# Optimization experiments

Hardware: AMD Instinct MI355X
Metric: run time of the kernel (lower is better)

## Reference

```python
import jax, jax.numpy as jnp
import numpy as np

SEQ_LEN = 2_097_152  # free sequence dimension
NUM_SYMBOLS = 10
NUM_STATES = 10
NUM_CLASSES = 2


def setup_inputs() -> dict:
    key = jax.random.key(0)
    k1, k2, k3, k4 = jax.random.split(key, 4)
    # x[t] is a probability distribution over symbols (soft one-hot), matching
    # the automaton semantics and keeping the 2M-step recurrence numerically stable.
    x = jax.random.uniform(k1, (SEQ_LEN, NUM_SYMBOLS), dtype=jnp.float32)
    x = x / jnp.sum(x, axis=1, keepdims=True)
    # Parameters, initialized exactly as in the torch module (__init__ softmaxes).
    P = jax.nn.softmax(jax.random.normal(k2, (NUM_SYMBOLS, NUM_STATES, NUM_STATES), dtype=jnp.float32), axis=2)
    start_state = jax.nn.softmax(jax.random.normal(k3, (NUM_STATES,), dtype=jnp.float32), axis=0)
    accept_states = jax.nn.softmax(jax.random.normal(k4, (NUM_STATES, NUM_CLASSES), dtype=jnp.float32), axis=1)
    return {"x": x, "P": P, "start_state": start_state, "accept_states": accept_states}


def reference(x, P, start_state, accept_states):
    # Sequential recurrence: s_{t+1} = s_t @ (sum_k x[t,k] * P[k])
    def step(s, xt):
        Wt = jnp.einsum('k,kij->ij', xt, P)  # [S, S] symbol-weighted transition
        return s @ Wt, None
    s, _ = jax.lax.scan(step, start_state, x)
    return s @ accept_states  # [num_classes]
```

## Files before the change

kernel.cpp:

```cpp
#include <hip/hip_runtime.h>

#define TEN 10

typedef float v2f __attribute__((ext_vector_type(2)));

#define PK_MUL_S0LO(d,s0,s1)   asm("v_pk_mul_f32 %0, %1, %2 op_sel:[0,0] op_sel_hi:[0,1]"         : "=v"(d)  : "v"(s0), "v"(s1))
#define PK_FMA_S0LO(acc,s0,s1) asm("v_pk_fma_f32 %0, %1, %2, %0 op_sel:[0,0,0] op_sel_hi:[0,1,1]" : "+v"(acc) : "v"(s0), "v"(s1))
#define PK_FMA_S0HI(acc,s0,s1) asm("v_pk_fma_f32 %0, %1, %2, %0 op_sel:[1,0,0] op_sel_hi:[1,1,1]" : "+v"(acc) : "v"(s0), "v"(s1))
#define PK_MUL_S1LO(d,s0,s1)   asm("v_pk_mul_f32 %0, %1, %2 op_sel:[0,0] op_sel_hi:[1,0]"         : "=v"(d)  : "v"(s0), "v"(s1))
#define PK_MUL_S1HI(d,s0,s1)   asm("v_pk_mul_f32 %0, %1, %2 op_sel:[0,1] op_sel_hi:[1,1]"         : "=v"(d)  : "v"(s0), "v"(s1))
#define PK_FMA_S1LO(acc,s0,s1) asm("v_pk_fma_f32 %0, %1, %2, %0 op_sel:[0,0,0] op_sel_hi:[1,0,1]" : "+v"(acc) : "v"(s0), "v"(s1))
#define PK_FMA_S1HI(acc,s0,s1) asm("v_pk_fma_f32 %0, %1, %2, %0 op_sel:[0,1,0] op_sel_hi:[1,1,1]" : "+v"(acc) : "v"(s0), "v"(s1))

__global__ __attribute__((amdgpu_flat_work_group_size(256, 256),
                          amdgpu_waves_per_eu(2, 2)))
void automaton_chunks(const float* __restrict__ x, const float* __restrict__ P,
                      float* __restrict__ outBlk, long long T, int C)
{
    __shared__ __align__(16) float lds[8704];

    const int tid  = threadIdx.x;
    const int wave = tid >> 6;
    const int lane = tid & 63;
    const int grp  = lane / 5;
    const int sub  = lane % 5;
    const bool active = (grp < 12);
    const int cib  = wave * 12 + grp;
    const int j0 = 2 * sub, j1 = j0 + 1;

    v2f p2[TEN][TEN];
    v2f m2[2][5];
    int Lc = 0;
    const v2f* xp = nullptr;
    float* slot = lds + (active ? cib : 0) * 132;
    float* wb0  = slot + j0 * 12;

    if (active) {
        const long long chunk = (long long)blockIdx.x * 48 + cib;
        const long long s0 = chunk * T / C;
        const long long s1 = (chunk + 1) * T / C;
        Lc = (int)(s1 - s0);
        xp = reinterpret_cast<const v2f*>(x) + s0 * 5;
#pragma unroll
        for (int k = 0; k < TEN; ++k)
#pragma unroll
            for (int a = 0; a < TEN; ++a) {
                const float2 v = *reinterpret_cast<const float2*>(P + k * 100 + a * TEN + j0);
                p2[k][a].x = v.x;
                p2[k][a].y = v.y;
            }
#pragma unroll
        for (int c = 0; c < 2; ++c)
#pragma unroll
            for (int i = 0; i < 5; ++i) {
                const int jc = 2 * sub + c;
                m2[c][i].x = (2 * i     == jc) ? 1.0f : 0.0f;
                m2[c][i].y = (2 * i + 1 == jc) ? 1.0f : 0.0f;
            }
    }

    v2f nxv0, nxv1, nxv2, nxv3, nxv4;
    if (active) {
        nxv0 = xp[0]; nxv1 = xp[1]; nxv2 = xp[2]; nxv3 = xp[3]; nxv4 = xp[4];
        xp += 5;
    }

    if (active) {
#pragma unroll 1
        for (int s = 0; s < Lc; ++s) {
            {
                *reinterpret_cast<v2f*>(wb0 + 0)  = m2[0][0];
                *reinterpret_cast<v2f*>(wb0 + 2)  = m2[0][1];
                *reinterpret_cast<v2f*>(wb0 + 4)  = m2[0][2];
                *reinterpret_cast<v2f*>(wb0 + 6)  = m2[0][3];
                *reinterpret_cast<v2f*>(wb0 + 8)  = m2[0][4];
                *reinterpret_cast<v2f*>(wb0 + 12) = m2[1][0];
                *reinterpret_cast<v2f*>(wb0 + 14) = m2[1][1];
                *reinterpret_cast<v2f*>(wb0 + 16) = m2[1][2];
                *reinterpret_cast<v2f*>(wb0 + 18) = m2[1][3];
                *reinterpret_cast<v2f*>(wb0 + 20) = m2[1][4];
            }
            __builtin_amdgcn_wave_barrier();

            v2f px0, px1, px2, px3, px4;
            if (s + 1 < Lc) {
                px0 = xp[0]; px1 = xp[1]; px2 = xp[2]; px3 = xp[3]; px4 = xp[4];
                xp += 5;
            }

#pragma unroll
            for (int a = 0; a < TEN; ++a) {
                union { float4 q; v2f h[2]; } u0, u1;
                union { float2 f; v2f v;   } u2;
                u0.q = *reinterpret_cast<const float4*>(slot + a * 12);
                u1.q = *reinterpret_cast<const float4*>(slot + a * 12 + 4);
                u2.f = *reinterpret_cast<const float2*>(slot + a * 12 + 8);
                const v2f c0 = u0.h[0], c1 = u0.h[1], c2 = u1.h[0], c3 = u1.h[1], c4 = u2.v;

                v2f w;
                PK_MUL_S0LO(w, nxv0, p2[0][a]);
                PK_FMA_S0HI(w, nxv0, p2[1][a]);
                PK_FMA_S0LO(w, nxv1, p2[2][a]);
                PK_FMA_S0HI(w, nxv1, p2[3][a]);
                PK_FMA_S0LO(w, nxv2, p2[4][a]);
                PK_FMA_S0HI(w, nxv2, p2[5][a]);
                PK_FMA_S0LO(w, nxv3, p2[6][a]);
                PK_FMA_S0HI(w, nxv3, p2[7][a]);
                PK_FMA_S0LO(w, nxv4, p2[8][a]);
                PK_FMA_S0HI(w, nxv4, p2[9][a]);

                if (a == 0) {
                    PK_MUL_S1LO(m2[0][0], c0, w);  PK_MUL_S1HI(m2[1][0], c0, w);
                    PK_MUL_S1LO(m2[0][1], c1, w);  PK_MUL_S1HI(m2[1][1], c1, w);
                    PK_MUL_S1LO(m2[0][2], c2, w);  PK_MUL_S1HI(m2[1][2], c2, w);
                    PK_MUL_S1LO(m2[0][3], c3, w);  PK_MUL_S1HI(m2[1][3], c3, w);
                    PK_MUL_S1LO(m2[0][4], c4, w);  PK_MUL_S1HI(m2[1][4], c4, w);
                } else {
                    PK_FMA_S1LO(m2[0][0], c0, w);  PK_FMA_S1HI(m2[1][0], c0, w);
                    PK_FMA_S1LO(m2[0][1], c1, w);  PK_FMA_S1HI(m2[1][1], c1, w);
                    PK_FMA_S1LO(m2[0][2], c2, w);  PK_FMA_S1HI(m2[1][2], c2, w);
                    PK_FMA_S1LO(m2[0][3], c3, w);  PK_FMA_S1HI(m2[1][3], c3, w);
                    PK_FMA_S1LO(m2[0][4], c4, w);  PK_FMA_S1HI(m2[1][4], c4, w);
                }
            }

            nxv0 = px0; nxv1 = px1; nxv2 = px2; nxv3 = px3; nxv4 = px4;
            __builtin_amdgcn_wave_barrier();
        }
    }

    __syncthreads();
    if (active) {
        float* t = lds + cib * 120;
#pragma unroll
        for (int i = 0; i < 5; ++i) {
            t[(2 * i)     * 12 + j0] = m2[0][i].x;
            t[(2 * i + 1) * 12 + j0] = m2[0][i].y;
            t[(2 * i)     * 12 + j1] = m2[1][i].x;
            t[(2 * i + 1) * 12 + j1] = m2[1][i].y;
        }
    }
    __syncthreads();

    {
        const float* src = lds;
        float* dst = lds + 5760;
        int n = 48;
        while (n > 3) {
            const int np = n >> 1;
            const int pI = tid / TEN;
            const int r  = tid % TEN;
            if (pI < np) {
                const float* A = src + (2 * pI) * 120;
                const float* B = src + (2 * pI + 1) * 120;
                float ar[TEN];
#pragma unroll
                for (int j = 0; j < TEN; ++j) ar[j] = A[r * 12 + j];
                float c[TEN] = {0, 0, 0, 0, 0, 0, 0, 0, 0, 0};
#pragma unroll
                for (int a = 0; a < TEN; ++a) {
                    const float ma = ar[a];
#pragma unroll
                    for (int j = 0; j < TEN; ++j) c[j] = fmaf(ma, B[a * 12 + j], c[j]);
                }
                float* Cp = dst + pI * 120;
#pragma unroll
                for (int j = 0; j < TEN; ++j) Cp[r * 12 + j] = c[j];
            }
            __syncthreads();
            const float* ts = src; src = dst; dst = const_cast<float*>(ts);
            n = np;
        }
        if (tid < TEN) {
            const int r = tid;
            float ar[TEN];
#pragma unroll
            for (int j = 0; j < TEN; ++j) ar[j] = src[r * 12 + j];
            float c[TEN] = {0, 0, 0, 0, 0, 0, 0, 0, 0, 0};
#pragma unroll
            for (int a = 0; a < TEN; ++a) {
                const float ma = ar[a];
#pragma unroll
                for (int j = 0; j < TEN; ++j) c[j] = fmaf(ma, src[120 + a * 12 + j], c[j]);
            }
#pragma unroll
            for (int j = 0; j < TEN; ++j) lds[5760 + r * 12 + j] = c[j];
        }
        __syncthreads();
        if (tid < TEN) {
            const int r = tid;
            float c[TEN] = {0, 0, 0, 0, 0, 0, 0, 0, 0, 0};
#pragma unroll
            for (int a = 0; a < TEN; ++a) {
                const float ma = lds[5760 + r * 12 + a];
#pragma unroll
                for (int j = 0; j < TEN; ++j) c[j] = fmaf(ma, src[240 + a * 12 + j], c[j]);
            }
            float* dr = outBlk + (size_t)blockIdx.x * 100 + r * TEN;
#pragma unroll
            for (int j = 0; j < TEN; ++j) dr[j] = c[j];
        }
    }
}

__device__ __forceinline__ void tree64(float* lds, int tid)
{
    const int q     = tid >> 2;
    const int sub   = tid & 3;
    const int rbase = (sub == 3) ? 8 : sub * 3;
    const int r0 = rbase, r1 = rbase + 1;
    const int r2 = (rbase + 2 > 9) ? 9 : rbase + 2;
    const bool w2 = (sub < 2);

    for (int np = 32; np >= 1; np >>= 1) {
        float c[3][TEN];
        if (q < np) {
            const float* A = lds + (2 * q) * 120;
            const float* B = lds + (2 * q + 1) * 120;
            float ar[3][TEN];
#pragma unroll
            for (int t = 0; t < 3; ++t) {
                const int rt = (t == 0) ? r0 : (t == 1) ? r1 : r2;
                const float4 a0 = reinterpret_cast<const float4*>(A + rt * 12)[0];
                const float4 a1 = reinterpret_cast<const float4*>(A + rt * 12)[1];
                const float2 a2 = reinterpret_cast<const float2*>(A + rt * 12 + 8)[0];
                ar[t][0]=a0.x; ar[t][1]=a0.y; ar[t][2]=a0.z; ar[t][3]=a0.w;
                ar[t][4]=a1.x; ar[t][5]=a1.y; ar[t][6]=a1.z; ar[t][7]=a1.w;
                ar[t][8]=a2.x; ar[t][9]=a2.y;
#pragma unroll
                for (int j = 0; j < TEN; ++j) c[t][j] = 0.0f;
            }
#pragma unroll
            for (int a = 0; a < TEN; ++a) {
                const float4 b0 = reinterpret_cast<const float4*>(B + a * 12)[0];
                const float4 b1 = reinterpret_cast<const float4*>(B + a * 12)[1];
                const float2 b2 = reinterpret_cast<const float2*>(B + a * 12 + 8)[0];
                const float br[TEN] = {b0.x,b0.y,b0.z,b0.w,b1.x,b1.y,b1.z,b1.w,b2.x,b2.y};
#pragma unroll
                for (int t = 0; t < 3; ++t) {
                    const float ma = ar[t][a];
#pragma unroll
                    for (int j = 0; j < TEN; ++j) c[t][j] = fmaf(ma, br[j], c[t][j]);
                }
            }
        }
        __syncthreads();
        if (q < np) {
            float* C = lds + q * 120;
#pragma unroll
            for (int t = 0; t < 3; ++t) {
                const int rt = (t == 0) ? r0 : (t == 1) ? r1 : r2;
                if (t < 2 || w2) {
                    float* cr = C + rt * 12;
                    reinterpret_cast<float4*>(cr)[0] = make_float4(c[t][0], c[t][1], c[t][2], c[t][3]);
                    reinterpret_cast<float4*>(cr)[1] = make_float4(c[t][4], c[t][5], c[t][6], c[t][7]);
                    reinterpret_cast<float2*>(cr + 8)[0] = make_float2(c[t][8], c[t][9]);
                }
            }
        }
        __syncthreads();
    }
}

__global__ void automaton_final(const float* __restrict__ blkM,
                                const float* __restrict__ start,
                                const float* __restrict__ acc,
                                float* __restrict__ outv)
{
    __shared__ __align__(16) float lds[7680];
    __shared__ float sv[TEN];
    const int tid = threadIdx.x;
    const int q   = tid >> 2;
    const int sub = tid & 3;
    const int rbase = (sub == 3) ? 8 : sub * 3;
    const int rr0 = rbase, rr1 = rbase + 1;
    const int rr2 = (rbase + 2 > 9) ? 9 : rbase + 2;
    const bool w2 = (sub < 2);

    float a[3][TEN];
    {
        const int rr[3] = {rr0, rr1, rr2};
        const float* A0 = blkM + (size_t)(8 * q) * 100;
#pragma unroll
        for (int t = 0; t < 3; ++t) {
            const float2* pp = reinterpret_cast<const float2*>(A0 + rr[t] * TEN);
            const float2 a0 = pp[0], a1 = pp[1], a2 = pp[2], a3 = pp[3], a4 = pp[4];
            a[t][0]=a0.x; a[t][1]=a0.y; a[t][2]=a1.x; a[t][3]=a1.y; a[t][4]=a2.x;
            a[t][5]=a2.y; a[t][6]=a3.x; a[t][7]=a3.y; a[t][8]=a4.x; a[t][9]=a4.y;
        }
    }
#pragma unroll 1
    for (int i = 1; i < 8; ++i) {
        const float* B = blkM + (size_t)(8 * q + i) * 100;
        float c[3][TEN];
#pragma unroll
        for (int t = 0; t < 3; ++t)
#pragma unroll
            for (int j = 0; j < TEN; ++j) c[t][j] = 0.0f;
#pragma unroll
        for (int aa = 0; aa < TEN; ++aa) {
            const float2* br = reinterpret_cast<const float2*>(B + aa * TEN);
            const float2 b0 = br[0], b1 = br[1], b2 = br[2], b3 = br[3], b4 = br[4];
            const float bv[TEN] = {b0.x,b0.y,b1.x,b1.y,b2.x,b2.y,b3.x,b3.y,b4.x,b4.y};
#pragma unroll
            for (int t = 0; t < 3; ++t) {
                const float ma = a[t][aa];
#pragma unroll
                for (int j = 0; j < TEN; ++j) c[t][j] = fmaf(ma, bv[j], c[t][j]);
            }
        }
#pragma unroll
        for (int t = 0; t < 3; ++t)
#pragma unroll
            for (int j = 0; j < TEN; ++j) a[t][j] = c[t][j];
    }
    {
        float* dst = lds + q * 120;
#pragma unroll
        for (int t = 0; t < 3; ++t) {
            const int rt = (t == 0) ? rr0 : (t == 1) ? rr1 : rr2;
            if (t < 2 || w2) {
                float* dr = dst + rt * 12;
                reinterpret_cast<float4*>(dr)[0] = make_float4(a[t][0], a[t][1], a[t][2], a[t][3]);
                reinterpret_cast<float4*>(dr)[1] = make_float4(a[t][4], a[t][5], a[t][6], a[t][7]);
                reinterpret_cast<float2*>(dr + 8)[0] = make_float2(a[t][8], a[t][9]);
            }
        }
    }
    __syncthreads();
    tree64(lds, tid);

    if (tid < TEN) {
        const int j = tid;
        float v = 0.0f;
#pragma unroll
        for (int r = 0; r < TEN; ++r) v = fmaf(start[r], lds[r * 12 + j], v);
        sv[j] = v;
    }
    __syncthreads();
    if (tid == 0) {
        float o0 = 0.0f, o1 = 0.0f;
#pragma unroll
        for (int j = 0; j < TEN; ++j) {
            o0 = fmaf(sv[j], acc[2 * j + 0], o0);
            o1 = fmaf(sv[j], acc[2 * j + 1], o1);
        }
        outv[0] = o0;
        outv[1] = o1;
    }
}

extern "C" void kernel_launch(void* const* d_in, const int* in_sizes, int n_in,
                              void* d_out, int out_size, void* d_ws, size_t ws_size,
                              hipStream_t stream)
{
    const float* x     = (const float*)d_in[0];
    const float* P     = (const float*)d_in[1];
    const float* start = (const float*)d_in[2];
    const float* acc   = (const float*)d_in[3];
    float* out         = (float*)d_out;

    const long long T = (long long)in_sizes[0] / TEN;
    const int C = 24576;

    float* blkM = (float*)d_ws;

    automaton_chunks<<<512, 256, 0, stream>>>(x, P, blkM, T, C);
    automaton_final<<<1, 256, 0, stream>>>(blkM, start, acc, out);
}
```

Baseline: 272.3 us.

## Fuse final reduction into chunk kernel via last-block atomic counter, double block size

```diff
diff --git a/kernel.cpp b/kernel.cpp
--- a/kernel.cpp
+++ b/kernel.cpp
@@ -12,12 +12,16 @@
 #define PK_FMA_S1LO(acc,s0,s1) asm("v_pk_fma_f32 %0, %1, %2, %0 op_sel:[0,0,0] op_sel_hi:[1,0,1]" : "+v"(acc) : "v"(s0), "v"(s1))
 #define PK_FMA_S1HI(acc,s0,s1) asm("v_pk_fma_f32 %0, %1, %2, %0 op_sel:[0,1,0] op_sel_hi:[1,1,1]" : "+v"(acc) : "v"(s0), "v"(s1))
 
-__global__ __attribute__((amdgpu_flat_work_group_size(256, 256),
+__global__ __attribute__((amdgpu_flat_work_group_size(512, 512),
                           amdgpu_waves_per_eu(2, 2)))
-void automaton_chunks(const float* __restrict__ x, const float* __restrict__ P,
-                      float* __restrict__ outBlk, long long T, int C)
+void automaton_fused(const float* __restrict__ x, const float* __restrict__ P,
+                     float* __restrict__ blkM,
+                     const float* __restrict__ start, const float* __restrict__ acc,
+                     float* __restrict__ outv, unsigned int* __restrict__ cnt,
+                     long long T, int C)
 {
-    __shared__ __align__(16) float lds[8704];
+    __shared__ __align__(16) float lds[17296];
+    __shared__ unsigned int oldc;
 
     const int tid  = threadIdx.x;
     const int wave = tid >> 6;
@@ -36,7 +40,7 @@
     float* wb0  = slot + j0 * 12;
 
     if (active) {
-        const long long chunk = (long long)blockIdx.x * 48 + cib;
+        const long long chunk = (long long)blockIdx.x * 96 + cib;
         const long long s0 = chunk * T / C;
         const long long s1 = (chunk + 1) * T / C;
         Lc = (int)(s1 - s0);
@@ -144,8 +148,8 @@
 
     {
         const float* src = lds;
-        float* dst = lds + 5760;
-        int n = 48;
+        float* dst = lds + 11520;
+        int n = 96;
         while (n > 3) {
             const int np = n >> 1;
             const int pI = tid / TEN;
@@ -171,6 +175,7 @@
             const float* ts = src; src = dst; dst = const_cast<float*>(ts);
             n = np;
         }
+        float* tmp = (src == lds) ? lds + 11520 : lds;
         if (tid < TEN) {
             const int r = tid;
             float ar[TEN];
@@ -184,7 +189,7 @@
                 for (int j = 0; j < TEN; ++j) c[j] = fmaf(ma, src[120 + a * 12 + j], c[j]);
             }
 #pragma unroll
-            for (int j = 0; j < TEN; ++j) lds[5760 + r * 12 + j] = c[j];
+            for (int j = 0; j < TEN; ++j) tmp[r * 12 + j] = c[j];
         }
         __syncthreads();
         if (tid < TEN) {
@@ -192,129 +197,69 @@
             float c[TEN] = {0, 0, 0, 0, 0, 0, 0, 0, 0, 0};
 #pragma unroll
             for (int a = 0; a < TEN; ++a) {
-                const float ma = lds[5760 + r * 12 + a];
+                const float ma = tmp[r * 12 + a];
 #pragma unroll
                 for (int j = 0; j < TEN; ++j) c[j] = fmaf(ma, src[240 + a * 12 + j], c[j]);
             }
-            float* dr = outBlk + (size_t)blockIdx.x * 100 + r * TEN;
+            float* dr = blkM + (size_t)blockIdx.x * 100 + r * TEN;
 #pragma unroll
             for (int j = 0; j < TEN; ++j) dr[j] = c[j];
         }
     }
-}
-
-__device__ __forceinline__ void tree64(float* lds, int tid)
-{
-    const int q     = tid >> 2;
-    const int sub   = tid & 3;
-    const int rbase = (sub == 3) ? 8 : sub * 3;
-    const int r0 = rbase, r1 = rbase + 1;
-    const int r2 = (rbase + 2 > 9) ? 9 : rbase + 2;
-    const bool w2 = (sub < 2);
-
-    for (int np = 32; np >= 1; np >>= 1) {
-        float c[3][TEN];
-        if (q < np) {
-            const float* A = lds + (2 * q) * 120;
-            const float* B = lds + (2 * q + 1) * 120;
-            float ar[3][TEN];
-#pragma unroll
-            for (int t = 0; t < 3; ++t) {
-                const int rt = (t == 0) ? r0 : (t == 1) ? r1 : r2;
-                const float4 a0 = reinterpret_cast<const float4*>(A + rt * 12)[0];
-                const float4 a1 = reinterpret_cast<const float4*>(A + rt * 12)[1];
-                const float2 a2 = reinterpret_cast<const float2*>(A + rt * 12 + 8)[0];
-                ar[t][0]=a0.x; ar[t][1]=a0.y; ar[t][2]=a0.z; ar[t][3]=a0.w;
-                ar[t][4]=a1.x; ar[t][5]=a1.y; ar[t][6]=a1.z; ar[t][7]=a1.w;
-                ar[t][8]=a2.x; ar[t][9]=a2.y;
-#pragma unroll
-                for (int j = 0; j < TEN; ++j) c[t][j] = 0.0f;
-            }
-#pragma unroll
-            for (int a = 0; a < TEN; ++a) {
-                const float4 b0 = reinterpret_cast<const float4*>(B + a * 12)[0];
-                const float4 b1 = reinterpret_cast<const float4*>(B + a * 12)[1];
-                const float2 b2 = reinterpret_cast<const float2*>(B + a * 12 + 8)[0];
-                const float br[TEN] = {b0.x,b0.y,b0.z,b0.w,b1.x,b1.y,b1.z,b1.w,b2.x,b2.y};
-#pragma unroll
-                for (int t = 0; t < 3; ++t) {
-                    const float ma = ar[t][a];
-#pragma unroll
-                    for (int j = 0; j < TEN; ++j) c[t][j] = fmaf(ma, br[j], c[t][j]);
-                }
-            }
-        }
-        __syncthreads();
-        if (q < np) {
-            float* C = lds + q * 120;
-#pragma unroll
-            for (int t = 0; t < 3; ++t) {
-                const int rt = (t == 0) ? r0 : (t == 1) ? r1 : r2;
-                if (t < 2 || w2) {
-                    float* cr = C + rt * 12;
-                    reinterpret_cast<float4*>(cr)[0] = make_float4(c[t][0], c[t][1], c[t][2], c[t][3]);
-                    reinterpret_cast<float4*>(cr)[1] = make_float4(c[t][4], c[t][5], c[t][6], c[t][7]);
-                    reinterpret_cast<float2*>(cr + 8)[0] = make_float2(c[t][8], c[t][9]);
-                }
-            }
-        }
-        __syncthreads();
-    }
-}
-
-__global__ void automaton_final(const float* __restrict__ blkM,
-                                const float* __restrict__ start,
-                                const float* __restrict__ acc,
-                                float* __restrict__ outv)
-{
-    __shared__ __align__(16) float lds[7680];
-    __shared__ float sv[TEN];
-    const int tid = threadIdx.x;
+
+    __threadfence();
+    __syncthreads();
+    if (tid == 0) oldc = atomicAdd(cnt, 1u);
+    __syncthreads();
+    if (oldc != (unsigned int)(gridDim.x - 1)) return;
+
+    __threadfence();
+
     const int q   = tid >> 2;
-    const int sub = tid & 3;
-    const int rbase = (sub == 3) ? 8 : sub * 3;
+    const int sub4 = tid & 3;
+    const int rbase = (sub4 == 3) ? 8 : sub4 * 3;
     const int rr0 = rbase, rr1 = rbase + 1;
     const int rr2 = (rbase + 2 > 9) ? 9 : rbase + 2;
-    const bool w2 = (sub < 2);
-
-    float a[3][TEN];
-    {
-        const int rr[3] = {rr0, rr1, rr2};
-        const float* A0 = blkM + (size_t)(8 * q) * 100;
-#pragma unroll
-        for (int t = 0; t < 3; ++t) {
-            const float2* pp = reinterpret_cast<const float2*>(A0 + rr[t] * TEN);
-            const float2 a0 = pp[0], a1 = pp[1], a2 = pp[2], a3 = pp[3], a4 = pp[4];
-            a[t][0]=a0.x; a[t][1]=a0.y; a[t][2]=a1.x; a[t][3]=a1.y; a[t][4]=a2.x;
-            a[t][5]=a2.y; a[t][6]=a3.x; a[t][7]=a3.y; a[t][8]=a4.x; a[t][9]=a4.y;
-        }
-    }
+    const bool w2 = (sub4 < 2);
+
+    if (tid < 256) {
+        float a[3][TEN];
+        {
+            const int rr[3] = {rr0, rr1, rr2};
+            const float* A0 = blkM + (size_t)(4 * q) * 100;
+#pragma unroll
+            for (int t = 0; t < 3; ++t) {
+                const float2* pp = reinterpret_cast<const float2*>(A0 + rr[t] * TEN);
+                const float2 a0 = pp[0], a1 = pp[1], a2 = pp[2], a3 = pp[3], a4 = pp[4];
+                a[t][0]=a0.x; a[t][1]=a0.y; a[t][2]=a1.x; a[t][3]=a1.y; a[t][4]=a2.x;
+                a[t][5]=a2.y; a[t][6]=a3.x; a[t][7]=a3.y; a[t][8]=a4.x; a[t][9]=a4.y;
+            }
+        }
 #pragma unroll 1
-    for (int i = 1; i < 8; ++i) {
-        const float* B = blkM + (size_t)(8 * q + i) * 100;
-        float c[3][TEN];
-#pragma unroll
-        for (int t = 0; t < 3; ++t)
-#pragma unroll
-            for (int j = 0; j < TEN; ++j) c[t][j] = 0.0f;
-#pragma unroll
-        for (int aa = 0; aa < TEN; ++aa) {
-            const float2* br = reinterpret_cast<const float2*>(B + aa * TEN);
-            const float2 b0 = br[0], b1 = br[1], b2 = br[2], b3 = br[3], b4 = br[4];
-            const float bv[TEN] = {b0.x,b0.y,b1.x,b1.y,b2.x,b2.y,b3.x,b3.y,b4.x,b4.y};
-#pragma unroll
-            for (int t = 0; t < 3; ++t) {
-                const float ma = a[t][aa];
-#pragma unroll
-                for (int j = 0; j < TEN; ++j) c[t][j] = fmaf(ma, bv[j], c[t][j]);
-            }
-        }
-#pragma unroll
-        for (int t = 0; t < 3; ++t)
-#pragma unroll
-            for (int j = 0; j < TEN; ++j) a[t][j] = c[t][j];
-    }
-    {
+        for (int i = 1; i < 4; ++i) {
+            const float* B = blkM + (size_t)(4 * q + i) * 100;
+            float c[3][TEN];
+#pragma unroll
+            for (int t = 0; t < 3; ++t)
+#pragma unroll
+                for (int j = 0; j < TEN; ++j) c[t][j] = 0.0f;
+#pragma unroll
+            for (int aa = 0; aa < TEN; ++aa) {
+                const float2* br = reinterpret_cast<const float2*>(B + aa * TEN);
+                const float2 b0 = br[0], b1 = br[1], b2 = br[2], b3 = br[3], b4 = br[4];
+                const float bv[TEN] = {b0.x,b0.y,b1.x,b1.y,b2.x,b2.y,b3.x,b3.y,b4.x,b4.y};
+#pragma unroll
+                for (int t = 0; t < 3; ++t) {
+                    const float ma = a[t][aa];
+#pragma unroll
+                    for (int j = 0; j < TEN; ++j) c[t][j] = fmaf(ma, bv[j], c[t][j]);
+                }
+            }
+#pragma unroll
+            for (int t = 0; t < 3; ++t)
+#pragma unroll
+                for (int j = 0; j < TEN; ++j) a[t][j] = c[t][j];
+        }
         float* dst = lds + q * 120;
 #pragma unroll
         for (int t = 0; t < 3; ++t) {
@@ -328,8 +273,58 @@
         }
     }
     __syncthreads();
-    tree64(lds, tid);
-
+
+    for (int np = 32; np >= 1; np >>= 1) {
+        float c[3][TEN];
+        const bool act = (q < np) && (tid < 256);
+        if (act) {
+            const float* A = lds + (2 * q) * 120;
+            const float* B = lds + (2 * q + 1) * 120;
+            float ar[3][TEN];
+#pragma unroll
+            for (int t = 0; t < 3; ++t) {
+                const int rt = (t == 0) ? rr0 : (t == 1) ? rr1 : rr2;
+                const float4 a0 = reinterpret_cast<const float4*>(A + rt * 12)[0];
+                const float4 a1 = reinterpret_cast<const float4*>(A + rt * 12)[1];
+                const float2 a2 = reinterpret_cast<const float2*>(A + rt * 12 + 8)[0];
+                ar[t][0]=a0.x; ar[t][1]=a0.y; ar[t][2]=a0.z; ar[t][3]=a0.w;
+                ar[t][4]=a1.x; ar[t][5]=a1.y; ar[t][6]=a1.z; ar[t][7]=a1.w;
+                ar[t][8]=a2.x; ar[t][9]=a2.y;
+#pragma unroll
+                for (int j = 0; j < TEN; ++j) c[t][j] = 0.0f;
+            }
+#pragma unroll
+            for (int a = 0; a < TEN; ++a) {
+                const float4 b0 = reinterpret_cast<const float4*>(B + a * 12)[0];
+                const float4 b1 = reinterpret_cast<const float4*>(B + a * 12)[1];
+                const float2 b2 = reinterpret_cast<const float2*>(B + a * 12 + 8)[0];
+                const float br[TEN] = {b0.x,b0.y,b0.z,b0.w,b1.x,b1.y,b1.z,b1.w,b2.x,b2.y};
+#pragma unroll
+                for (int t = 0; t < 3; ++t) {
+                    const float ma = ar[t][a];
+#pragma unroll
+                    for (int j = 0; j < TEN; ++j) c[t][j] = fmaf(ma, br[j], c[t][j]);
+                }
+            }
+        }
+        __syncthreads();
+        if (act) {
+            float* C = lds + q * 120;
+#pragma unroll
+            for (int t = 0; t < 3; ++t) {
+                const int rt = (t == 0) ? rr0 : (t == 1) ? rr1 : rr2;
+                if (t < 2 || w2) {
+                    float* cr = C + rt * 12;
+                    reinterpret_cast<float4*>(cr)[0] = make_float4(c[t][0], c[t][1], c[t][2], c[t][3]);
+                    reinterpret_cast<float4*>(cr)[1] = make_float4(c[t][4], c[t][5], c[t][6], c[t][7]);
+                    reinterpret_cast<float2*>(cr + 8)[0] = make_float2(c[t][8], c[t][9]);
+                }
+            }
+        }
+        __syncthreads();
+    }
+
+    float* sv = lds + 17280;
     if (tid < TEN) {
         const int j = tid;
         float v = 0.0f;
@@ -364,7 +359,8 @@
     const int C = 24576;
 
     float* blkM = (float*)d_ws;
-
-    automaton_chunks<<<512, 256, 0, stream>>>(x, P, blkM, T, C);
-    automaton_final<<<1, 256, 0, stream>>>(blkM, start, acc, out);
+    unsigned int* cnt = (unsigned int*)((char*)d_ws + 256 * 100 * sizeof(float));
+
+    hipMemsetAsync(cnt, 0, sizeof(unsigned int), stream);
+    automaton_fused<<<256, 512, 0, stream>>>(x, P, blkM, start, acc, out, cnt, T, C);
 }
```

Result: slower. 296.7 us (+9.0%).
